# Kernel optimization log

Hardware: AMD Instinct MI355X
Metric: run time of the kernel (lower is better)

Reference implementation:

```python
import jax, jax.numpy as jnp
import numpy as np

N_NODES = 50000


def setup_inputs() -> dict:
    key = jax.random.key(0)
    k1, k2, k3, k4, k5 = jax.random.split(key, 5)
    N, E, D_IN, D_OUT = N_NODES, 800000, 128, 128
    features = jax.random.normal(k1, (N, D_IN), dtype=jnp.float32)
    src = jax.random.randint(k2, (E,), 0, N, dtype=jnp.int32)
    dst = jax.random.randint(k3, (E,), 0, N, dtype=jnp.int32)
    # Kaiming-ish init for linear weights
    W_self = jax.random.normal(k4, (D_IN, D_OUT), dtype=jnp.float32) / np.sqrt(D_IN)
    W_neigh = jax.random.normal(k5, (D_IN, D_OUT), dtype=jnp.float32) / np.sqrt(D_IN)
    b = jnp.zeros((D_OUT,), dtype=jnp.float32)
    return {"features": features, "src": src, "dst": dst,
            "W_self": W_self, "W_neigh": W_neigh, "b": b}


def reference(features, src, dst, W_self, W_neigh, b):
    # DGL SAGEConv with 'mean' aggregator:
    #   h_neigh[v] = mean_{(u->v) in E} features[u]   (0 if in-degree 0)
    #   out = features @ W_self + h_neigh @ W_neigh + b
    N = features.shape[0]
    # gather source features along edges, then segment-sum into destinations
    neigh_sum = jax.ops.segment_sum(features[src], dst, num_segments=N)  # [N, D]
    deg = jax.ops.segment_sum(jnp.ones_like(dst, dtype=features.dtype), dst,
                              num_segments=N)  # [N]
    h_neigh = neigh_sum / jnp.maximum(deg, 1.0)[:, None]
    return features @ W_self + h_neigh @ W_neigh + b
```

## Files before the change

### kernel.cpp

```cpp
#include <hip/hip_runtime.h>

#define D 128
#define EC 4096
#define BSH 8
#define CAP 5120

typedef __attribute__((ext_vector_type(8))) short bf16x8;
typedef __attribute__((ext_vector_type(4))) float f32x4;

__device__ __forceinline__ unsigned short f2bf(float f) {
    union { float f; unsigned int u; } c;
    c.f = f;
    unsigned int lsb = (c.u >> 16) & 1u;
    c.u += 0x7fffu + lsb;
    return (unsigned short)(c.u >> 16);
}

__device__ __forceinline__ float bf_lo(unsigned int x) {
    union { unsigned int u; float f; } c;
    c.u = x << 16;
    return c.f;
}
__device__ __forceinline__ float bf_hi(unsigned int x) {
    union { unsigned int u; float f; } c;
    c.u = x & 0xffff0000u;
    return c.f;
}

__global__ __launch_bounds__(256) void prep_kernel(const float* __restrict__ feat,
                                                   unsigned short* __restrict__ fb,
                                                   const float* __restrict__ Ws,
                                                   const float* __restrict__ Wn,
                                                   unsigned short* __restrict__ Wfrag,
                                                   int* __restrict__ bin_cursor,
                                                   int castB, int n8) {
    int bid = blockIdx.x;
    int t   = threadIdx.x;
    if (bid < castB) {
        int i = bid * 256 + t;
        if (i >= n8) return;
        const float4* s = (const float4*)(feat + (size_t)i * 8);
        float4 a = s[0];
        float4 b = s[1];
        unsigned short pk[8];
        pk[0] = f2bf(a.x); pk[1] = f2bf(a.y); pk[2] = f2bf(a.z); pk[3] = f2bf(a.w);
        pk[4] = f2bf(b.x); pk[5] = f2bf(b.y); pk[6] = f2bf(b.z); pk[7] = f2bf(b.w);
        *(bf16x8*)(fb + (size_t)i * 8) = *(const bf16x8*)pk;
    } else if (bid < castB + 16) {
        int tid = (bid - castB) * 256 + t;
        int l  = tid & 63;
        int ks = (tid >> 6) & 7;
        int nt = tid >> 9;
        int n  = nt * 16 + (l & 15);
        int kb = ks * 32 + (l >> 4) * 8;
        unsigned short pk[8];
#pragma unroll
        for (int j = 0; j < 8; ++j) {
            int k = kb + j;
            float w = (k < 128) ? Ws[k * D + n] : Wn[(k - 128) * D + n];
            pk[j] = f2bf(w);
        }
        *(bf16x8*)(Wfrag + (size_t)tid * 8) = *(const bf16x8*)pk;
    } else {
        bin_cursor[t] = 0;
    }
}

__global__ __launch_bounds__(256) void binscatter_kernel(const int* __restrict__ src,
                                                         const int* __restrict__ dst,
                                                         int* __restrict__ bin_cursor,
                                                         unsigned int* __restrict__ ebuf,
                                                         int E, int NB) {
    __shared__ int cnt[256];
    __shared__ int basev[256];
    __shared__ int cur[256];
    int t = threadIdx.x;
    cnt[t] = 0;
    cur[t] = 0;
    __syncthreads();
    int base = blockIdx.x * EC;
#pragma unroll
    for (int i = 0; i < EC / 256; ++i) {
        int e = base + i * 256 + t;
        if (e < E) atomicAdd(&cnt[dst[e] >> BSH], 1);
    }
    __syncthreads();
    if (t < NB && cnt[t]) basev[t] = atomicAdd(&bin_cursor[t], cnt[t]);
    __syncthreads();
#pragma unroll
    for (int i = 0; i < EC / 256; ++i) {
        int e = base + i * 256 + t;
        if (e < E) {
            int d = dst[e];
            int b = d >> BSH;
            int loc = basev[b] + atomicAdd(&cur[b], 1);
            if (loc < CAP)
                ebuf[(size_t)b * CAP + loc] =
                    (unsigned int)src[e] | ((unsigned int)(d & ((1 << BSH) - 1)) << 16);
        }
    }
}

__global__ __launch_bounds__(256) void csrbin_kernel(const unsigned int* __restrict__ ebuf,
                                                     const int* __restrict__ bin_cursor,
                                                     int* __restrict__ rs_g,
                                                     int* __restrict__ deg_g,
                                                     unsigned short* __restrict__ bucket,
                                                     int N) {
    __shared__ int degL[256];
    __shared__ int scn[256];
    __shared__ int cur[256];
    int b = blockIdx.x;
    int t = threadIdx.x;
    int cntb = bin_cursor[b];
    if (cntb > CAP) cntb = CAP;
    int s  = b * CAP;
    int e2 = s + cntb;

    degL[t] = 0;
    cur[t]  = 0;
    __syncthreads();
    for (int i = s + t; i < e2; i += 256)
        atomicAdd(&degL[(ebuf[i] >> 16) & 255], 1);
    __syncthreads();

    int v = degL[t];
    scn[t] = v;
    __syncthreads();
    for (int off = 1; off < 256; off <<= 1) {
        int add = (t >= off) ? scn[t - off] : 0;
        __syncthreads();
        scn[t] += add;
        __syncthreads();
    }

    for (int i = s + t; i < e2; i += 256) {
        unsigned int p = ebuf[i];
        int dl = (p >> 16) & 255;
        int sl = atomicAdd(&cur[dl], 1);
        bucket[s + (scn[dl] - degL[dl]) + sl] = (unsigned short)(p & 0xffffu);
    }
    __syncthreads();

    int node = (b << BSH) + t;
    if (node < N) {
        rs_g[node]  = s + scn[t] - degL[t];
        deg_g[node] = degL[t];
    }
}

__global__ __launch_bounds__(256) void gather_kernel(const unsigned short* __restrict__ fb,
                                                     const unsigned short* __restrict__ bucket,
                                                     const int* __restrict__ rs,
                                                     const int* __restrict__ deg,
                                                     unsigned short* __restrict__ hb, int N) {
    int wid  = (blockIdx.x * 256 + threadIdx.x) >> 6;
    int lane = threadIdx.x & 63;
    if (wid >= N) return;
    int v    = wid;
    int d    = deg[v];
    int base = rs[v];
    int g = lane >> 4;
    int c = lane & 15;

    float acc[8];
#pragma unroll
    for (int j = 0; j < 8; ++j) acc[j] = 0.f;

    int u0 = (g < d)     ? (int)bucket[base + g]     : 0;
    int u1 = (g + 4 < d) ? (int)bucket[base + g + 4] : 0;
    for (int i = g; i < d; i += 8) {
        int n0 = (i + 8  < d) ? (int)bucket[base + i + 8]  : 0;
        int n1 = (i + 12 < d) ? (int)bucket[base + i + 12] : 0;
        uint4 x0 = *(const uint4*)(fb + (size_t)u0 * D + c * 8);
        acc[0] += bf_lo(x0.x); acc[1] += bf_hi(x0.x);
        acc[2] += bf_lo(x0.y); acc[3] += bf_hi(x0.y);
        acc[4] += bf_lo(x0.z); acc[5] += bf_hi(x0.z);
        acc[6] += bf_lo(x0.w); acc[7] += bf_hi(x0.w);
        if (i + 4 < d) {
            uint4 x1 = *(const uint4*)(fb + (size_t)u1 * D + c * 8);
            acc[0] += bf_lo(x1.x); acc[1] += bf_hi(x1.x);
            acc[2] += bf_lo(x1.y); acc[3] += bf_hi(x1.y);
            acc[4] += bf_lo(x1.z); acc[5] += bf_hi(x1.z);
            acc[6] += bf_lo(x1.w); acc[7] += bf_hi(x1.w);
        }
        u0 = n0; u1 = n1;
    }

#pragma unroll
    for (int j = 0; j < 8; ++j) {
        acc[j] += __shfl_xor(acc[j], 16);
        acc[j] += __shfl_xor(acc[j], 32);
    }

    if (g == 0) {
        float inv = (d > 0) ? 1.0f / (float)d : 0.0f;
        unsigned short pk[8];
#pragma unroll
        for (int j = 0; j < 8; ++j) pk[j] = f2bf(acc[j] * inv);
        *(bf16x8*)(hb + (size_t)v * D + c * 8) = *(const bf16x8*)pk;
    }
}

__global__ __launch_bounds__(256) void out_mfma_kernel(const unsigned short* __restrict__ fb,
                                                       const unsigned short* __restrict__ hb,
                                                       const unsigned short* __restrict__ Wfrag,
                                                       const float* __restrict__ bias,
                                                       float* __restrict__ out, int N) {
    int t    = threadIdx.x;
    int w    = t >> 6;
    int lane = t & 63;
    int lo16 = lane & 15;
    int quad = lane >> 4;
    int v0   = blockIdx.x * 64;

    int rowA = v0 + w * 16 + lo16;
    if (rowA > N - 1) rowA = N - 1;

    f32x4 acc[8];
#pragma unroll
    for (int nt = 0; nt < 8; ++nt) acc[nt] = (f32x4){0.f, 0.f, 0.f, 0.f};

#pragma unroll
    for (int ks = 0; ks < 8; ++ks) {
        const unsigned short* xsrc = (ks < 4)
            ? fb + (size_t)rowA * D + ks * 32 + quad * 8
            : hb + (size_t)rowA * D + (ks - 4) * 32 + quad * 8;
        bf16x8 a = *(const bf16x8*)xsrc;
        const unsigned short* wp = Wfrag + ((size_t)ks * 64 + lane) * 8;
#pragma unroll
        for (int nt = 0; nt < 8; ++nt) {
            bf16x8 b = *(const bf16x8*)(wp + (size_t)nt * 4096);
            acc[nt] = __builtin_amdgcn_mfma_f32_16x16x32_bf16(a, b, acc[nt], 0, 0, 0);
        }
    }

#pragma unroll
    for (int nt = 0; nt < 8; ++nt) {
        int n = nt * 16 + lo16;
        float bv = bias[n];
#pragma unroll
        for (int r = 0; r < 4; ++r) {
            int row = v0 + w * 16 + quad * 4 + r;
            if (row < N) out[(size_t)row * D + n] = acc[nt][r] + bv;
        }
    }
}

extern "C" void kernel_launch(void* const* d_in, const int* in_sizes, int n_in,
                              void* d_out, int out_size, void* d_ws, size_t ws_size,
                              hipStream_t stream) {
    const float* feat = (const float*)d_in[0];
    const int*   src  = (const int*)d_in[1];
    const int*   dst  = (const int*)d_in[2];
    const float* Ws   = (const float*)d_in[3];
    const float* Wn   = (const float*)d_in[4];
    const float* bias = (const float*)d_in[5];
    float*       out  = (float*)d_out;

    const int N  = in_sizes[0] / D;
    const int E  = in_sizes[1];
    const int NB = (N + (1 << BSH) - 1) >> BSH;
    const int nchunk = (E + EC - 1) / EC;
    const int castB  = (N * D / 8 + 255) / 256;

    int* bin_cursor = (int*)d_ws;
    int* rs         = bin_cursor + 256;
    int* deg        = rs + N;
    unsigned int* ebuf = (unsigned int*)(deg + N);
    unsigned short* bucket = (unsigned short*)(ebuf + (size_t)NB * CAP);
    size_t short_count = (size_t)NB * CAP;
    short_count = (short_count + 7) & ~(size_t)7;
    unsigned short* fb    = bucket + short_count;
    unsigned short* hb    = fb + (size_t)N * D;
    unsigned short* Wfrag = hb + (size_t)N * D;

    prep_kernel<<<castB + 17, 256, 0, stream>>>(feat, fb, Ws, Wn, Wfrag, bin_cursor,
                                                castB, N * D / 8);
    binscatter_kernel<<<nchunk, 256, 0, stream>>>(src, dst, bin_cursor, ebuf, E, NB);
    csrbin_kernel<<<NB, 256, 0, stream>>>(ebuf, bin_cursor, rs, deg, bucket, N);
    gather_kernel<<<(N * 64 + 255) / 256, 256, 0, stream>>>(fb, bucket, rs, deg, hb, N);
    out_mfma_kernel<<<(N + 63) / 64, 256, 0, stream>>>(fb, hb, Wfrag, bias, out, N);
}
```

Baseline: 176.2 us.

## Fuse neighbor mean gather into MFMA output kernel via LDS staging

```diff
diff --git a/kernel.cpp b/kernel.cpp
--- a/kernel.cpp
+++ b/kernel.cpp
@@ -4,6 +4,7 @@
 #define EC 4096
 #define BSH 8
 #define CAP 5120
+#define HPAD 136
 
 typedef __attribute__((ext_vector_type(8))) short bf16x8;
 typedef __attribute__((ext_vector_type(4))) float f32x4;
@@ -149,100 +150,128 @@
     }
 }
 
-__global__ __launch_bounds__(256) void gather_kernel(const unsigned short* __restrict__ fb,
-                                                     const unsigned short* __restrict__ bucket,
-                                                     const int* __restrict__ rs,
-                                                     const int* __restrict__ deg,
-                                                     unsigned short* __restrict__ hb, int N) {
-    int wid  = (blockIdx.x * 256 + threadIdx.x) >> 6;
-    int lane = threadIdx.x & 63;
-    if (wid >= N) return;
-    int v    = wid;
-    int d    = deg[v];
-    int base = rs[v];
-    int g = lane >> 4;
-    int c = lane & 15;
-
-    float acc[8];
-#pragma unroll
-    for (int j = 0; j < 8; ++j) acc[j] = 0.f;
-
-    int u0 = (g < d)     ? (int)bucket[base + g]     : 0;
-    int u1 = (g + 4 < d) ? (int)bucket[base + g + 4] : 0;
-    for (int i = g; i < d; i += 8) {
-        int n0 = (i + 8  < d) ? (int)bucket[base + i + 8]  : 0;
-        int n1 = (i + 12 < d) ? (int)bucket[base + i + 12] : 0;
-        uint4 x0 = *(const uint4*)(fb + (size_t)u0 * D + c * 8);
-        acc[0] += bf_lo(x0.x); acc[1] += bf_hi(x0.x);
-        acc[2] += bf_lo(x0.y); acc[3] += bf_hi(x0.y);
-        acc[4] += bf_lo(x0.z); acc[5] += bf_hi(x0.z);
-        acc[6] += bf_lo(x0.w); acc[7] += bf_hi(x0.w);
-        if (i + 4 < d) {
-            uint4 x1 = *(const uint4*)(fb + (size_t)u1 * D + c * 8);
-            acc[0] += bf_lo(x1.x); acc[1] += bf_hi(x1.x);
-            acc[2] += bf_lo(x1.y); acc[3] += bf_hi(x1.y);
-            acc[4] += bf_lo(x1.z); acc[5] += bf_hi(x1.z);
-            acc[6] += bf_lo(x1.w); acc[7] += bf_hi(x1.w);
-        }
-        u0 = n0; u1 = n1;
-    }
-
-#pragma unroll
-    for (int j = 0; j < 8; ++j) {
-        acc[j] += __shfl_xor(acc[j], 16);
-        acc[j] += __shfl_xor(acc[j], 32);
-    }
-
-    if (g == 0) {
-        float inv = (d > 0) ? 1.0f / (float)d : 0.0f;
-        unsigned short pk[8];
-#pragma unroll
-        for (int j = 0; j < 8; ++j) pk[j] = f2bf(acc[j] * inv);
-        *(bf16x8*)(hb + (size_t)v * D + c * 8) = *(const bf16x8*)pk;
-    }
-}
-
-__global__ __launch_bounds__(256) void out_mfma_kernel(const unsigned short* __restrict__ fb,
-                                                       const unsigned short* __restrict__ hb,
-                                                       const unsigned short* __restrict__ Wfrag,
-                                                       const float* __restrict__ bias,
-                                                       float* __restrict__ out, int N) {
+__global__ __launch_bounds__(256) void gather_mfma_kernel(
+        const unsigned short* __restrict__ fb,
+        const unsigned short* __restrict__ bucket,
+        const int* __restrict__ rs,
+        const int* __restrict__ deg,
+        const unsigned short* __restrict__ Wfrag,
+        const float* __restrict__ bias,
+        float* __restrict__ out, int N) {
+    __shared__ unsigned short hL[64 * HPAD];
+
     int t    = threadIdx.x;
     int w    = t >> 6;
     int lane = t & 63;
     int lo16 = lane & 15;
     int quad = lane >> 4;
+    int g    = quad;
+    int c    = lo16;
     int v0   = blockIdx.x * 64;
+
+    int nidx = v0 + w * 16 + lo16;
+    int ncl  = (nidx < N) ? nidx : N - 1;
+    int dv   = deg[ncl];
+    int bv   = rs[ncl];
+
+    for (int nn = 0; nn < 16; ++nn) {
+        int node = v0 + w * 16 + nn;
+        int d    = __shfl(dv, nn);
+        int base = __shfl(bv, nn);
+
+        float acc[8];
+#pragma unroll
+        for (int j = 0; j < 8; ++j) acc[j] = 0.f;
+
+        if (node < N) {
+            int u0 = (g < d)      ? (int)bucket[base + g]      : 0;
+            int u1 = (g + 4 < d)  ? (int)bucket[base + g + 4]  : 0;
+            int u2 = (g + 8 < d)  ? (int)bucket[base + g + 8]  : 0;
+            int u3 = (g + 12 < d) ? (int)bucket[base + g + 12] : 0;
+            for (int i = g; i < d; i += 16) {
+                int n0 = (i + 16 < d) ? (int)bucket[base + i + 16] : 0;
+                int n1 = (i + 20 < d) ? (int)bucket[base + i + 20] : 0;
+                int n2 = (i + 24 < d) ? (int)bucket[base + i + 24] : 0;
+                int n3 = (i + 28 < d) ? (int)bucket[base + i + 28] : 0;
+                bool b1 = (i + 4 < d), b2 = (i + 8 < d), b3 = (i + 12 < d);
+                uint4 x0 = *(const uint4*)(fb + (size_t)u0 * D + c * 8);
+                uint4 x1, x2, x3;
+                if (b1) x1 = *(const uint4*)(fb + (size_t)u1 * D + c * 8);
+                if (b2) x2 = *(const uint4*)(fb + (size_t)u2 * D + c * 8);
+                if (b3) x3 = *(const uint4*)(fb + (size_t)u3 * D + c * 8);
+                acc[0] += bf_lo(x0.x); acc[1] += bf_hi(x0.x);
+                acc[2] += bf_lo(x0.y); acc[3] += bf_hi(x0.y);
+                acc[4] += bf_lo(x0.z); acc[5] += bf_hi(x0.z);
+                acc[6] += bf_lo(x0.w); acc[7] += bf_hi(x0.w);
+                if (b1) {
+                    acc[0] += bf_lo(x1.x); acc[1] += bf_hi(x1.x);
+                    acc[2] += bf_lo(x1.y); acc[3] += bf_hi(x1.y);
+                    acc[4] += bf_lo(x1.z); acc[5] += bf_hi(x1.z);
+                    acc[6] += bf_lo(x1.w); acc[7] += bf_hi(x1.w);
+                }
+                if (b2) {
+                    acc[0] += bf_lo(x2.x); acc[1] += bf_hi(x2.x);
+                    acc[2] += bf_lo(x2.y); acc[3] += bf_hi(x2.y);
+                    acc[4] += bf_lo(x2.z); acc[5] += bf_hi(x2.z);
+                    acc[6] += bf_lo(x2.w); acc[7] += bf_hi(x2.w);
+                }
+                if (b3) {
+                    acc[0] += bf_lo(x3.x); acc[1] += bf_hi(x3.x);
+                    acc[2] += bf_lo(x3.y); acc[3] += bf_hi(x3.y);
+                    acc[4] += bf_lo(x3.z); acc[5] += bf_hi(x3.z);
+                    acc[6] += bf_lo(x3.w); acc[7] += bf_hi(x3.w);
+                }
+                u0 = n0; u1 = n1; u2 = n2; u3 = n3;
+            }
+        }
+
+#pragma unroll
+        for (int j = 0; j < 8; ++j) {
+            acc[j] += __shfl_xor(acc[j], 16);
+            acc[j] += __shfl_xor(acc[j], 32);
+        }
+
+        if (g == 0) {
+            float inv = (node < N && d > 0) ? 1.0f / (float)d : 0.0f;
+            unsigned short pk[8];
+#pragma unroll
+            for (int j = 0; j < 8; ++j) pk[j] = f2bf(acc[j] * inv);
+            *(bf16x8*)&hL[(w * 16 + nn) * HPAD + c * 8] = *(const bf16x8*)pk;
+        }
+    }
+    __syncthreads();
 
     int rowA = v0 + w * 16 + lo16;
     if (rowA > N - 1) rowA = N - 1;
-
-    f32x4 acc[8];
-#pragma unroll
-    for (int nt = 0; nt < 8; ++nt) acc[nt] = (f32x4){0.f, 0.f, 0.f, 0.f};
+    int lrow = w * 16 + lo16;
+
+    f32x4 accO[8];
+#pragma unroll
+    for (int nt = 0; nt < 8; ++nt) accO[nt] = (f32x4){0.f, 0.f, 0.f, 0.f};
 
 #pragma unroll
     for (int ks = 0; ks < 8; ++ks) {
-        const unsigned short* xsrc = (ks < 4)
-            ? fb + (size_t)rowA * D + ks * 32 + quad * 8
-            : hb + (size_t)rowA * D + (ks - 4) * 32 + quad * 8;
-        bf16x8 a = *(const bf16x8*)xsrc;
+        bf16x8 a;
+        if (ks < 4)
+            a = *(const bf16x8*)(fb + (size_t)rowA * D + ks * 32 + quad * 8);
+        else
+            a = *(const bf16x8*)&hL[lrow * HPAD + (ks - 4) * 32 + quad * 8];
         const unsigned short* wp = Wfrag + ((size_t)ks * 64 + lane) * 8;
 #pragma unroll
         for (int nt = 0; nt < 8; ++nt) {
             bf16x8 b = *(const bf16x8*)(wp + (size_t)nt * 4096);
-            acc[nt] = __builtin_amdgcn_mfma_f32_16x16x32_bf16(a, b, acc[nt], 0, 0, 0);
+            accO[nt] = __builtin_amdgcn_mfma_f32_16x16x32_bf16(a, b, accO[nt], 0, 0, 0);
         }
     }
 
 #pragma unroll
     for (int nt = 0; nt < 8; ++nt) {
         int n = nt * 16 + lo16;
-        float bv = bias[n];
+        float bvl = bias[n];
 #pragma unroll
         for (int r = 0; r < 4; ++r) {
             int row = v0 + w * 16 + quad * 4 + r;
-            if (row < N) out[(size_t)row * D + n] = acc[nt][r] + bv;
+            if (row < N) out[(size_t)row * D + n] = accO[nt][r] + bvl;
         }
     }
 }
@@ -272,13 +301,12 @@
     size_t short_count = (size_t)NB * CAP;
     short_count = (short_count + 7) & ~(size_t)7;
     unsigned short* fb    = bucket + short_count;
-    unsigned short* hb    = fb + (size_t)N * D;
-    unsigned short* Wfrag = hb + (size_t)N * D;
+    unsigned short* Wfrag = fb + (size_t)N * D;
 
     prep_kernel<<<castB + 17, 256, 0, stream>>>(feat, fb, Ws, Wn, Wfrag, bin_cursor,
                                                 castB, N * D / 8);
     binscatter_kernel<<<nchunk, 256, 0, stream>>>(src, dst, bin_cursor, ebuf, E, NB);
     csrbin_kernel<<<NB, 256, 0, stream>>>(ebuf, bin_cursor, rs, deg, bucket, N);
-    gather_kernel<<<(N * 64 + 255) / 256, 256, 0, stream>>>(fb, bucket, rs, deg, hb, N);
-    out_mfma_kernel<<<(N + 63) / 64, 256, 0, stream>>>(fb, hb, Wfrag, bias, out, N);
-}
+    gather_mfma_kernel<<<(N + 63) / 64, 256, 0, stream>>>(fb, bucket, rs, deg, Wfrag,
+                                                          bias, out, N);
+}
```

After: 176.2 us. About the same (-0.0%).
